# Kernel tuning notes

Hardware: AMD Instinct MI355X
Metric: run time of the kernel (lower is better)

## Reference

```python
import jax, jax.numpy as jnp
import numpy as np

DIL = 1  # dilation (== padding for 3x3 stride-1)
KK = 9   # 3x3 kernel points


def setup_inputs() -> dict:
    key = jax.random.key(0)
    k1, k2, k3, k4 = jax.random.split(key, 4)
    B, C, H, W = 8, 64, 128, 128
    Cout = 64
    x = jax.random.normal(k1, (B, C, H, W), jnp.float32)
    # offset/mask conv: nn.Conv2d default init scale-ish; keep offsets moderate
    w_off = jax.random.normal(k2, (27, C, 3, 3), jnp.float32) * 0.02
    b_off = jax.random.uniform(k3, (27,), jnp.float32, -0.05, 0.05)
    # c2_msra_fill: std = sqrt(2 / (fan_in + fan_out)), fan_in = C*9
    std = float(np.sqrt(2.0 / (C * 9 + Cout)))
    w_dcn = jax.random.normal(k4, (Cout, C, 3, 3), jnp.float32) * std
    return {"x": x, "w_off": w_off, "b_off": b_off, "w_dcn": w_dcn}


def _conv3x3(x, w, b, dil):
    out = jax.lax.conv_general_dilated(
        x, w, window_strides=(1, 1), padding=[(dil, dil), (dil, dil)],
        rhs_dilation=(dil, dil), dimension_numbers=("NCHW", "OIHW", "NCHW"))
    return out + b[None, :, None, None]


def reference(x, w_off, b_off, w_dcn):
    B, C, H, W = x.shape
    Cout = w_dcn.shape[0]
    # offset/mask conv, chunk into offset_x / offset_y / mask, cat offsets
    om = _conv3x3(x, w_off, b_off, DIL)                  # [B,27,H,W]
    off_x, off_y, mask = jnp.split(om, 3, axis=1)        # each [B,9,H,W]
    offset = jnp.concatenate([off_x, off_y], axis=1)     # [B,18,H,W]
    mask = jax.nn.sigmoid(mask)                          # [B,9,H,W]
    # mmcv DCNv2 layout: offset channel 2k = dy_k, 2k+1 = dx_k
    off = offset.reshape(B, KK, 2, H, W)
    dy, dx = off[:, :, 0], off[:, :, 1]                  # [B,9,H,W]
    # base sampling grid: p = out_pos - pad + k*dil (stride 1, pad = dil)
    ky, kx = jnp.meshgrid(jnp.arange(3), jnp.arange(3), indexing="ij")
    ky = ky.reshape(KK).astype(jnp.float32)
    kx = kx.reshape(KK).astype(jnp.float32)
    base_y = (jnp.arange(H, dtype=jnp.float32)[None, :, None]
              - DIL + ky[:, None, None] * DIL)           # [9,H,1]
    base_x = (jnp.arange(W, dtype=jnp.float32)[None, None, :]
              - DIL + kx[:, None, None] * DIL)           # [9,1,W]
    py = dy + base_y[None]                               # [B,9,H,W]
    px = dx + base_x[None]
    # bilinear sample with zero padding outside the image
    y0 = jnp.floor(py)
    x0 = jnp.floor(px)
    xf = x.reshape(B, C, H * W)
    sampled = jnp.zeros((B, C, KK, H, W), x.dtype)
    for oy in (0.0, 1.0):
        for ox in (0.0, 1.0):
            yi = y0 + oy
            xi = x0 + ox
            wgt = (1.0 - jnp.abs(py - yi)) * (1.0 - jnp.abs(px - xi))
            valid = (yi >= 0) & (yi < H) & (xi >= 0) & (xi < W)
            yc = jnp.clip(yi, 0, H - 1).astype(jnp.int32)
            xc = jnp.clip(xi, 0, W - 1).astype(jnp.int32)
            idx = (yc * W + xc).reshape(B, KK * H * W)
            vals = jax.vmap(lambda f, i: jnp.take(f, i, axis=1))(xf, idx)
            vals = vals.reshape(B, C, KK, H, W)
            sampled = sampled + vals * (wgt * valid)[:, None]
    sampled = sampled * mask[:, None]                    # modulation
    # weighted reduction == conv with gathered patches
    out = jnp.einsum("bckhw,ock->bohw", sampled, w_dcn.reshape(Cout, C, KK))
    return out
```

## Files before the change

kernel.cpp:

```cpp
#include <hip/hip_runtime.h>
#include <math.h>

#define B_  8
#define C_  64
#define H_  128
#define W_  128
#define KK_ 9
#define CO_ 64
#define HW_ (H_*W_)
#define CK_ 576

typedef _Float16 f16x8 __attribute__((ext_vector_type(8)));
typedef _Float16 h2    __attribute__((ext_vector_type(2)));
typedef __attribute__((ext_vector_type(4))) float f32x4;

__device__ inline unsigned pkrtz(float a, float b){
    auto v = __builtin_amdgcn_cvt_pkrtz(a, b);
    union{decltype(v) h; unsigned u;} c; c.h = v; return c.u;
}
__device__ inline h2 u2h(unsigned u){ union{unsigned x; h2 h;} c; c.x = u; return c.h; }
__device__ inline unsigned h2u(h2 v){ union{h2 h; unsigned u;} c; c.h = v; return c.u; }
__device__ inline unsigned short f2h(float f){
    _Float16 h = (_Float16)f;
    union{_Float16 h; unsigned short s;} c; c.h = h; return c.s;
}
__device__ inline h2 bcast_lo(unsigned u){ return u2h(__builtin_amdgcn_perm(u, u, 0x01000100)); }
__device__ inline h2 bcast_hi(unsigned u){ return u2h(__builtin_amdgcn_perm(u, u, 0x03020302)); }

__global__ __launch_bounds__(256) void transpose_prep(
    const float* __restrict__ x, unsigned short* __restrict__ xt,
    const float* __restrict__ w_dcn, const float* __restrict__ w_off,
    unsigned short* __restrict__ w_bf, unsigned short* __restrict__ wA)
{
    __shared__ unsigned tb[64 * 33];
    if (blockIdx.x >= B_ * 256) {
        int i = (blockIdx.x - B_ * 256) * 256 + threadIdx.x;
        if (i < 64 * CK_) {
            int o = i / CK_, r = i % CK_;
            int tap = r >> 6, c = r & 63;
            w_bf[i] = f2h(w_dcn[o * CK_ + c * 9 + tap]);
        } else {
            int j = i - 64 * CK_;
            int o = j / CK_, r = j % CK_;
            int tap = r >> 6, c = r & 63;
            float v = (o < 27) ? w_off[o * CK_ + c * 9 + tap] : 0.f;
            wA[j] = f2h(v);
        }
        return;
    }
    int b = blockIdx.x >> 8;
    int pixbase = (blockIdx.x & 255) * 64;
    int t = threadIdx.x;
    #pragma unroll
    for (int i = 0; i < 2; ++i) {
        int idx = i * 256 + t;
        int cp = idx >> 4;
        int p4 = (idx & 15) * 4;
        const float* r0 = x + ((size_t)(b * C_) + 2 * cp    ) * HW_ + pixbase + p4;
        const float* r1 = x + ((size_t)(b * C_) + 2 * cp + 1) * HW_ + pixbase + p4;
        float4 f0 = *(const float4*)r0;
        float4 f1 = *(const float4*)r1;
        tb[(p4 + 0) * 33 + cp] = pkrtz(f0.x, f1.x);
        tb[(p4 + 1) * 33 + cp] = pkrtz(f0.y, f1.y);
        tb[(p4 + 2) * 33 + cp] = pkrtz(f0.z, f1.z);
        tb[(p4 + 3) * 33 + cp] = pkrtz(f0.w, f1.w);
    }
    __syncthreads();
    unsigned* xo = (unsigned*)xt + ((size_t)b * HW_ + pixbase) * 32;
    #pragma unroll
    for (int i = 0; i < 2; ++i) {
        int idx = i * 256 + t;
        int pix = idx >> 3, j = idx & 7;
        uint4 v;
        v.x = tb[pix * 33 + j * 4 + 0];
        v.y = tb[pix * 33 + j * 4 + 1];
        v.z = tb[pix * 33 + j * 4 + 2];
        v.w = tb[pix * 33 + j * 4 + 3];
        *(uint4*)(xo + pix * 32 + j * 4) = v;
    }
}


#define PXB 144
#define ROWB (66 * PXB)

__global__ __launch_bounds__(256) void dcn_p1b(
    const unsigned short* __restrict__ xt,
    const unsigned short* __restrict__ wA,
    const float* __restrict__ b_off,
    uint4* __restrict__ scr_ws)
{
    __shared__ __align__(16) unsigned char xrow[3 * ROWB];
    float* om = (float*)xrow;

    int tile = blockIdx.x;
    int b  = tile >> 8;
    int p0 = (tile & 255) * 64;
    int y  = p0 >> 7;
    int x0 = p0 & 127;
    int t  = threadIdx.x;
    int lane = t & 63, w = t >> 6;
    int m = lane & 15, q = lane >> 4;

    const unsigned short* xbr = xt + (size_t)(b * HW_) * 64;

    for (int i = t; i < 3 * 66 * 8; i += 256) {
        int r = i / 528;
        int rem = i - r * 528;
        int c = rem >> 3;
        int g = rem & 7;
        int yy = y - 1 + r;
        int xx = x0 - 1 + c;
        uint4 v = {0, 0, 0, 0};
        if (yy >= 0 && yy < H_ && xx >= 0 && xx < W_)
            v = *(const uint4*)(xbr + ((size_t)yy * W_ + xx) * 64 + g * 8);
        *(uint4*)(xrow + r * ROWB + c * PXB + g * 16) = v;
    }
    __syncthreads();

    {
        int o0c = (w & 1) * 16;
        int pxh = (w >> 1) * 32;

        f32x4 accc[2] = {};
        #pragma unroll
        for (int ky = 0; ky < 3; ++ky) {
            #pragma unroll
            for (int kx = 0; kx < 3; ++kx) {
                int s2 = (ky * 3 + kx) * 2;
                f16x8 A0 = *(const f16x8*)(wA + (o0c + m) * CK_ + s2 * 32 + q * 8);
                f16x8 A1 = *(const f16x8*)(wA + (o0c + m) * CK_ + (s2 + 1) * 32 + q * 8);
                #pragma unroll
                for (int nt = 0; nt < 2; ++nt) {
                    int c = pxh + nt * 16 + m + kx;
                    const unsigned char* p = xrow + ky * ROWB + c * PXB + q * 16;
                    f16x8 b0 = *(const f16x8*)p;
                    f16x8 b1 = *(const f16x8*)(p + 64);
                    accc[nt] = __builtin_amdgcn_mfma_f32_16x16x32_f16(A0, b0, accc[nt], 0, 0, 0);
                    accc[nt] = __builtin_amdgcn_mfma_f32_16x16x32_f16(A1, b1, accc[nt], 0, 0, 0);
                }
            }
        }
        __syncthreads();
        #pragma unroll
        for (int nt = 0; nt < 2; ++nt) {
            #pragma unroll
            for (int r = 0; r < 4; ++r) {
                int j = o0c + q * 4 + r;
                if (j < 27)
                    om[j * 65 + pxh + nt * 16 + m] = accc[nt][r] + b_off[j];
            }
        }
    }
    __syncthreads();

    uint4* srow = scr_ws + (size_t)tile * 576;
    for (int i = t; i < 576; i += 256) {
        int k = i >> 6, sp = i & 63;
        float dy = om[(2 * k)     * 65 + sp];
        float dx = om[(2 * k + 1) * 65 + sp];
        float mk = 1.f / (1.f + __expf(-om[(18 + k) * 65 + sp]));
        float py = dy + (float)(y - 1 + k / 3);
        float px = dx + (float)(x0 + sp - 1 + k % 3);
        float fy = floorf(py), fx = floorf(px);
        int iy = (int)fy, ix = (int)fx;
        float ay = py - fy, ax = px - fx;
        float wy0 = (iy >= 0  && iy < H_)     ? (1.f - ay) : 0.f;
        float wy1 = (iy >= -1 && iy < H_ - 1) ? ay         : 0.f;
        float wx0 = (ix >= 0  && ix < W_)     ? (1.f - ax) : 0.f;
        float wx1 = (ix >= -1 && ix < W_ - 1) ? ax         : 0.f;
        int iy0 = min(max(iy, 0), H_ - 1);
        int iy1 = min(max(iy + 1, 0), H_ - 1);
        int ix0 = min(max(ix, 0), W_ - 1);
        int ix1 = min(max(ix + 1, 0), W_ - 1);
        float w00 = wy0*wx0*mk, w01 = wy0*wx1*mk, w10 = wy1*wx0*mk, w11 = wy1*wx1*mk;
        uint4 rec;
        rec.x = pkrtz(w00, w01);
        rec.y = pkrtz(w10, w11);
        int off00 = (iy0 * W_ + ix0) * 128;
        rec.z = (unsigned)(off00 | ((ix1 != ix0) << 22) | ((iy1 != iy0) << 23));
        rec.w = 0;
        srow[i] = rec;
    }
}

#define SSTR4 400
__global__ __launch_bounds__(256, 4) void dcn_p2(
    const unsigned short* __restrict__ xt,
    const unsigned short* __restrict__ w_bf,
    const uint4* __restrict__ scr_ws,
    float* __restrict__ out)
{
    __shared__ __align__(16) unsigned char sS[64 * SSTR4];
    __shared__ uint2 scr_w[576];
    __shared__ int   scr_o[576];

    int tile = blockIdx.x;
    int b  = tile >> 8;
    int p0 = (tile & 255) * 64;
    int t  = threadIdx.x;
    int lane = t & 63, w = t >> 6;
    int m = lane & 15, q = lane >> 4;

    const unsigned short* xbr = xt + (size_t)(b * HW_) * 64;

    const uint4* srow = scr_ws + (size_t)tile * 576;
    for (int i = t; i < 576; i += 256) {
        uint4 rec = srow[i];
        scr_w[i] = (uint2){rec.x, rec.y};
        scr_o[i] = (int)rec.z;
    }
    int o0 = w * 16;
    __syncthreads();

    int cq = lane & 7;
    int g  = lane >> 3;
    const unsigned char* xb = (const unsigned char*)xbr;
    f32x4 acc[4] = {};
    int piB = w * 8 + g;

    uint2 wA_, wB_; int pB_;
    uint4 a00, a01, a10, a11;
    {
        wA_ = scr_w[piB];      int oo = scr_o[piB];
        wB_ = scr_w[piB + 32]; pB_ = scr_o[piB + 32];
        const unsigned char* a0 = xb + (oo & 0x3FFFFF) + cq * 16;
        int dxb = (oo >> 15) & 128;
        int dyb = (oo >> 9)  & 16384;
        a00 = *(const uint4*)(a0);
        a01 = *(const uint4*)(a0 + dxb);
        a10 = *(const uint4*)(a0 + dyb);
        a11 = *(const uint4*)(a0 + dyb + dxb);
    }

    #pragma unroll
    for (int chunk = 0; chunk < 3; ++chunk) {
        #pragma unroll
        for (int it6 = 0; it6 < 6; ++it6) {
            const int k = chunk * 6 + it6;
            uint2 wC_ = {}; int pC_ = 0;
            if (k + 2 < 18) {
                int P = piB + (k + 2) * 32;
                wC_ = scr_w[P]; pC_ = scr_o[P];
            }
            uint4 n00 = {}, n01 = {}, n10 = {}, n11 = {};
            if (k + 1 < 18) {
                const unsigned char* a0 = xb + (pB_ & 0x3FFFFF) + cq * 16;
                int dxb = (pB_ >> 15) & 128;
                int dyb = (pB_ >> 9)  & 16384;
                n00 = *(const uint4*)(a0);
                n01 = *(const uint4*)(a0 + dxb);
                n10 = *(const uint4*)(a0 + dyb);
                n11 = *(const uint4*)(a0 + dyb + dxb);
            }
            h2 w00 = bcast_lo(wA_.x), w01 = bcast_hi(wA_.x);
            h2 w10 = bcast_lo(wA_.y), w11 = bcast_hi(wA_.y);
            uint4 o4; h2 r;
            r = w00*u2h(a00.x) + w01*u2h(a01.x) + w10*u2h(a10.x) + w11*u2h(a11.x); o4.x = h2u(r);
            r = w00*u2h(a00.y) + w01*u2h(a01.y) + w10*u2h(a10.y) + w11*u2h(a11.y); o4.y = h2u(r);
            r = w00*u2h(a00.z) + w01*u2h(a01.z) + w10*u2h(a10.z) + w11*u2h(a11.z); o4.z = h2u(r);
            r = w00*u2h(a00.w) + w01*u2h(a01.w) + w10*u2h(a10.w) + w11*u2h(a11.w); o4.w = h2u(r);
            int sp  = (piB + (k & 1) * 32) & 63;
            int ktl = it6 >> 1;
            *(uint4*)&sS[sp * SSTR4 + ktl * 128 + cq * 16] = o4;
            wA_ = wB_; wB_ = wC_; pB_ = pC_;
            a00 = n00; a01 = n01; a10 = n10; a11 = n11;
        }
        f16x8 Af[6];
        #pragma unroll
        for (int s = 0; s < 6; ++s)
            Af[s] = *(const f16x8*)(w_bf + (o0 + m) * CK_ + (chunk * 6 + s) * 32 + q * 8);
        __syncthreads();

        #pragma unroll
        for (int s = 0; s < 6; ++s) {
            #pragma unroll
            for (int nt = 0; nt < 4; ++nt) {
                f16x8 bb = *(const f16x8*)&sS[(nt * 16 + m) * SSTR4 + s * 64 + q * 16];
                acc[nt] = __builtin_amdgcn_mfma_f32_16x16x32_f16(Af[s], bb, acc[nt], 0, 0, 0);
            }
        }
        __syncthreads();
    }

    #pragma unroll
    for (int nt = 0; nt < 4; ++nt) {
        #pragma unroll
        for (int r = 0; r < 4; ++r) {
            int o = o0 + q * 4 + r;
            out[((size_t)(b * CO_ + o)) * HW_ + p0 + nt * 16 + m] = acc[nt][r];
        }
    }
}

extern "C" void kernel_launch(void* const* d_in, const int* in_sizes, int n_in,
                              void* d_out, int out_size, void* d_ws, size_t ws_size,
                              hipStream_t stream)
{
    const float* x     = (const float*)d_in[0];
    const float* w_off = (const float*)d_in[1];
    const float* b_off = (const float*)d_in[2];
    const float* w_dcn = (const float*)d_in[3];
    float* out = (float*)d_out;

    unsigned short* xt   = (unsigned short*)d_ws;
    unsigned short* w_bf = xt + (size_t)B_ * HW_ * 64;
    unsigned short* wA   = w_bf + 64 * CK_;
    uint4* scr_ws = (uint4*)(wA + 32 * CK_);

    transpose_prep<<<B_ * 256 + 216, 256, 0, stream>>>(x, xt, w_dcn, w_off, w_bf, wA);
    dcn_p1b<<<B_ * 256, 256, 0, stream>>>(xt, wA, b_off, scr_ws);
    dcn_p2<<<B_ * 256, 256, 0, stream>>>(xt, w_bf, scr_ws, out);
}
```

Measured before the change: 161.1 us.

## Fuse offset/mask conv kernel with deformable sampling GEMM kernel

Merges the offset-conv/sampling-record kernel and the deformable gather+MFMA kernel into one kernel. Sampling weights and offsets go straight to shared memory instead of a global scratch buffer that was written and then re-read. The sampling tile reuses the input-row LDS region. This removes one launch and the global scratch round trip, at the cost of higher per-block LDS and register pressure under the 4-block launch bound.

```diff
diff --git a/kernel.cpp b/kernel.cpp
--- a/kernel.cpp
+++ b/kernel.cpp
@@ -83,15 +83,20 @@
 
 #define PXB 144
 #define ROWB (66 * PXB)
-
-__global__ __launch_bounds__(256) void dcn_p1b(
+#define SSTR4 400
+
+__global__ __launch_bounds__(256, 4) void dcn15(
     const unsigned short* __restrict__ xt,
     const unsigned short* __restrict__ wA,
     const float* __restrict__ b_off,
-    uint4* __restrict__ scr_ws)
+    const unsigned short* __restrict__ w_bf,
+    float* __restrict__ out)
 {
     __shared__ __align__(16) unsigned char xrow[3 * ROWB];
+    __shared__ uint2 scr_w[576];
+    __shared__ int   scr_o[576];
     float* om = (float*)xrow;
+    unsigned char* sS = xrow;
 
     int tile = blockIdx.x;
     int b  = tile >> 8;
@@ -154,7 +159,6 @@
     }
     __syncthreads();
 
-    uint4* srow = scr_ws + (size_t)tile * 576;
     for (int i = t; i < 576; i += 256) {
         int k = i >> 6, sp = i & 63;
         float dy = om[(2 * k)     * 65 + sp];
@@ -174,42 +178,14 @@
         int ix0 = min(max(ix, 0), W_ - 1);
         int ix1 = min(max(ix + 1, 0), W_ - 1);
         float w00 = wy0*wx0*mk, w01 = wy0*wx1*mk, w10 = wy1*wx0*mk, w11 = wy1*wx1*mk;
-        uint4 rec;
-        rec.x = pkrtz(w00, w01);
-        rec.y = pkrtz(w10, w11);
+        uint2 wv;
+        wv.x = pkrtz(w00, w01);
+        wv.y = pkrtz(w10, w11);
+        scr_w[i] = wv;
         int off00 = (iy0 * W_ + ix0) * 128;
-        rec.z = (unsigned)(off00 | ((ix1 != ix0) << 22) | ((iy1 != iy0) << 23));
-        rec.w = 0;
-        srow[i] = rec;
-    }
-}
-
-#define SSTR4 400
-__global__ __launch_bounds__(256, 4) void dcn_p2(
-    const unsigned short* __restrict__ xt,
-    const unsigned short* __restrict__ w_bf,
-    const uint4* __restrict__ scr_ws,
-    float* __restrict__ out)
-{
-    __shared__ __align__(16) unsigned char sS[64 * SSTR4];
-    __shared__ uint2 scr_w[576];
-    __shared__ int   scr_o[576];
-
-    int tile = blockIdx.x;
-    int b  = tile >> 8;
-    int p0 = (tile & 255) * 64;
-    int t  = threadIdx.x;
-    int lane = t & 63, w = t >> 6;
-    int m = lane & 15, q = lane >> 4;
-
-    const unsigned short* xbr = xt + (size_t)(b * HW_) * 64;
-
-    const uint4* srow = scr_ws + (size_t)tile * 576;
-    for (int i = t; i < 576; i += 256) {
-        uint4 rec = srow[i];
-        scr_w[i] = (uint2){rec.x, rec.y};
-        scr_o[i] = (int)rec.z;
-    }
+        scr_o[i] = off00 | ((ix1 != ix0) << 22) | ((iy1 != iy0) << 23);
+    }
+
     int o0 = w * 16;
     __syncthreads();
 
@@ -306,9 +282,7 @@
     unsigned short* xt   = (unsigned short*)d_ws;
     unsigned short* w_bf = xt + (size_t)B_ * HW_ * 64;
     unsigned short* wA   = w_bf + 64 * CK_;
-    uint4* scr_ws = (uint4*)(wA + 32 * CK_);
 
     transpose_prep<<<B_ * 256 + 216, 256, 0, stream>>>(x, xt, w_dcn, w_off, w_bf, wA);
-    dcn_p1b<<<B_ * 256, 256, 0, stream>>>(xt, wA, b_off, scr_ws);
-    dcn_p2<<<B_ * 256, 256, 0, stream>>>(xt, w_bf, scr_ws, out);
-}
+    dcn15<<<B_ * 256, 256, 0, stream>>>(xt, wA, b_off, w_bf, out);
+}
```

Measured after the change: 145.9 us. -9.4%, faster.
